# Optimization experiments

Measured on AMD Instinct MI355X. Metric: run time of the kernel, lower is better.

Reference implementation:

```python
import jax, jax.numpy as jnp
import numpy as np
import itertools

# ---- fixed problem dims ----
B, C, G, D, H, W_SP = 2, 32, 24, 24, 24, 24   # octahedral group |G| = 24 (isomorphic to S4)
N_SEL = 3                                      # selective bispectrum: 2nd shift restricted to {e, transposition, 4-cycle}
FEAT = G * N_SEL                               # 72 invariant features per channel
HEAD = 64


def _octahedral_tables():
    """Cayley table of the octahedral rotation group (== S4) and the selective generator set."""
    perms = list(itertools.permutations(range(4)))          # lexicographic; identity at index 0
    idx = {p: i for i, p in enumerate(perms)}
    # cayley[i, j] = index of p_i o p_j, with (p o q)(k) = p(q(k))
    cay = np.array([[idx[tuple(p[q[k]] for k in range(4))] for q in perms] for p in perms],
                   dtype=np.int32)
    sel = np.array([idx[(0, 1, 2, 3)],   # identity
                    idx[(1, 0, 2, 3)],   # transposition (generator)
                    idx[(1, 2, 3, 0)]],  # 4-cycle (generator)
                   dtype=np.int32)
    return cay, sel


def setup_inputs() -> dict:
    key = jax.random.key(0)
    k1, k2, k3 = jax.random.split(key, 3)
    x = jax.random.normal(k1, (B, C, G, D, H, W_SP), dtype=jnp.float32)
    cay, sel = _octahedral_tables()
    # 1x1x1 Conv3d params: weight (HEAD, C*FEAT), bias (HEAD,)
    fan_in = C * FEAT
    W = jax.random.normal(k2, (HEAD, fan_in), dtype=jnp.float32) * (1.0 / np.sqrt(fan_in))
    b = jax.random.normal(k3, (HEAD,), dtype=jnp.float32) * 0.01
    return {"x": x, "W": W, "b": b,
            "cayley": jnp.asarray(cay), "sel_idx": jnp.asarray(sel)}


def _bispectrum_pool(x, W, b, cayley, sel_idx):
    Bb, Cc, Gg, Dd, Hh, Ww = x.shape
    # (B,C,G,D,H,W) -> rows of group signals, one per (b,c,voxel)
    xf = x.astype(jnp.float32).transpose(0, 1, 3, 4, 5, 2).reshape(-1, Gg)   # (N, 24)
    N = xf.shape[0]
    # Selective triple correlation (bispectrum in group domain):
    #   tau[n, h, s] = sum_g f(g) * f(g.h) * f(g.s),  s in selective generator set
    tau = jnp.zeros((N, Gg, N_SEL), dtype=jnp.float32)
    for g in range(Gg):                      # fixed small loop over 24 group elements
        row = cayley[g]                      # (24,) indices of g.h for all h
        fgh = xf[:, row]                     # (N, 24)
        fgs = fgh[:, sel_idx]                # (N, 3)
        tau = tau + xf[:, g][:, None, None] * fgh[:, :, None] * fgs[:, None, :]
    beta = tau.reshape(N, FEAT)              # real part of the bispectrum
    # sign * log1p compression
    out = jnp.sign(beta) * jnp.log1p(jnp.abs(beta))
    # (N, FEAT) -> (B, C*FEAT, D, H, W), channel index = c*FEAT + f (matches torch permute/reshape)
    out = out.reshape(Bb, Cc, Dd, Hh, Ww, FEAT).transpose(0, 1, 5, 2, 3, 4)
    out = out.reshape(Bb, Cc * FEAT, Dd, Hh, Ww)
    out = jax.nn.relu(out)
    # 1x1x1 conv == per-voxel GEMM
    y = jnp.einsum('bkdhw,ok->bodhw', out, W) + b[None, :, None, None, None]
    return y


def reference(x, W, b, cayley, sel_idx):
    return _bispectrum_pool(x, W, b, cayley, sel_idx)
```

## Files before the change

kernel.cpp:

```cpp
#include <hip/hip_runtime.h>
#include <stdint.h>

#define DHW         13824
#define NCH         32
#define NG          24
#define KDIM        2304
#define NHEAD       64
#define TP          16
#define CHS         16
#define FPC         64
#define KP2         2048
#define KS2         64
#define KPSTG       32
#define KQ          8
#define KPE         1032
#define TILES_PER_B 864
#define NTILES      1728
#define OUTN        1769472
#define PREPB       512
#define FILLB       1728

typedef __attribute__((ext_vector_type(2))) float    f32x2;
typedef __attribute__((ext_vector_type(8))) short    s16x8;
typedef __attribute__((ext_vector_type(4))) float    f32x4;
typedef __attribute__((ext_vector_type(4))) uint32_t u32x4;

struct Tables { int cay[NG][NG]; int s1[NG]; int s2[NG]; int t1h[NG]; int rep[12]; };

constexpr Tables make_tables() {
    int perms[NG][4] = {};
    int n = 0;
    for (int a = 0; a < 4; ++a)
        for (int b = 0; b < 4; ++b) {
            if (b == a) continue;
            for (int c = 0; c < 4; ++c) {
                if (c == a || c == b) continue;
                int d = 6 - a - b - c;
                perms[n][0] = a; perms[n][1] = b; perms[n][2] = c; perms[n][3] = d;
                ++n;
            }
        }
    int si1 = 0, si2 = 0;
    for (int i = 0; i < NG; ++i) {
        if (perms[i][0] == 1 && perms[i][1] == 0 && perms[i][2] == 2 && perms[i][3] == 3) si1 = i;
        if (perms[i][0] == 1 && perms[i][1] == 2 && perms[i][2] == 3 && perms[i][3] == 0) si2 = i;
    }
    Tables t{};
    for (int p = 0; p < NG; ++p) {
        for (int q = 0; q < NG; ++q) {
            int c0 = perms[p][perms[q][0]];
            int c1 = perms[p][perms[q][1]];
            int c2 = perms[p][perms[q][2]];
            int c3 = perms[p][perms[q][3]];
            int r = 0;
            for (int i = 0; i < NG; ++i)
                if (perms[i][0] == c0 && perms[i][1] == c1 &&
                    perms[i][2] == c2 && perms[i][3] == c3) { r = i; break; }
            t.cay[p][q] = r;
        }
        t.s1[p] = t.cay[p][si1];
        t.s2[p] = t.cay[p][si2];
    }
    for (int h = 0; h < NG; ++h) t.t1h[h] = t.cay[si1][h];
    int nr = 0;
    for (int h = 0; h < NG; ++h) if (h < t.t1h[h]) t.rep[nr++] = h;
    return t;
}
constexpr Tables TAB = make_tables();

__device__ __forceinline__ uint32_t f2bf(float f) {
    uint32_t u = __float_as_uint(f);
    u += 0x7fffu + ((u >> 16) & 1u);
    return u >> 16;
}

__global__ __launch_bounds__(256) void init_all(const float* __restrict__ W,
                                                unsigned short* __restrict__ WbS,
                                                const float* __restrict__ bias,
                                                float* __restrict__ y) {
    const int blk = blockIdx.x;
    if (blk < PREPB) {
        int i = blk * 256 + threadIdx.x;
        int j  = i & 7;
        int t1_ = i >> 3;
        int l  = t1_ & 63;
        int t2_ = t1_ >> 6;
        int kk = t2_ & (KS2 - 1);
        int ot = t2_ >> 6;
        int o = ot * 16 + (l & 15);
        int k = kk * 32 + ((l >> 4) << 3) + j;
        int stage = k >> 10;
        int q     = k & 1023;
        int c = stage * CHS + (q >> 6);
        int f = q & 63;
        const float* Wo = W + o * KDIM + c * 72;
        float val = 0.f;
        if (f < 24)      val = Wo[f * 3 + 0];
        else if (f < 36) { int h = TAB.rep[f - 24];
                           val = Wo[h * 3 + 1] + Wo[TAB.t1h[h] * 3 + 1]; }
        else if (f < 60) { int h = f - 36;          val = Wo[h * 3 + 2]; }
        WbS[i] = (unsigned short)f2bf(val * 0.69314718055994531f);
    } else {
        const int i4 = (blk - PREPB) * 256 + threadIdx.x;
        const float b = bias[((i4 * 4) / DHW) & (NHEAD - 1)];
        f32x4 v; v[0] = b; v[1] = b; v[2] = b; v[3] = b;
        ((f32x4*)y)[i4] = v;
    }
}

__global__ __launch_bounds__(256, 2)
void bispec_fused(
        const float* __restrict__ x,
        const unsigned short* __restrict__ WbS,
        float* __restrict__ y)
{
    __shared__ alignas(16) unsigned short featS[TP * KPE];

    const int bid = blockIdx.x;
    const int NB  = NTILES * 2;
    const int swz   = (bid & 7) * (NB / 8) + (bid >> 3);
    const int tile  = swz % NTILES;
    const int stage = swz / NTILES;
    const int bb  = tile / TILES_PER_B;
    const int psp = (tile - bb * TILES_PER_B) * TP;
    const int tid = threadIdx.x;

    const int p0 = tid & 15;
    const int cl = tid >> 4;
    const int w  = tid >> 6;
    const int l  = tid & 63;
    const int ln = l & 15;
    const int lh = l >> 4;

    f32x4 accA = {0.f, 0.f, 0.f, 0.f};
    f32x4 accB = {0.f, 0.f, 0.f, 0.f};
    f32x4 accC = {0.f, 0.f, 0.f, 0.f};
    f32x4 accD = {0.f, 0.f, 0.f, 0.f};

    {
        const int c0 = stage * CHS + cl;
        const unsigned idx0 = (unsigned)(bb * NCH + c0) * (NG * DHW) + (unsigned)(psp + p0);
        float xf[NG];
        #pragma unroll
        for (int g = 0; g < NG; ++g) xf[g] = x[idx0 + (unsigned)(g * DHW)];

        f32x2 tau02[NG];
        float tau1[12];
        #pragma unroll
        for (int h = 0; h < NG; ++h) tau02[h] = (f32x2){0.f, 0.f};
        #pragma unroll
        for (int r = 0; r < 12; ++r) tau1[r] = 0.f;
        #pragma unroll
        for (int g = 0; g < NG; ++g) {
            const float xg = xf[g];
            const f32x2 q02 = (f32x2){xg, xg} * (f32x2){xg, xf[TAB.s2[g]]};
            const float q1 = xg * xf[TAB.s1[g]];
            #pragma unroll
            for (int h = 0; h < NG; ++h) {
                const float v = xf[TAB.cay[g][h]];
                tau02[h] = __builtin_elementwise_fma((f32x2){v, v}, q02, tau02[h]);
            }
            #pragma unroll
            for (int r = 0; r < 12; ++r) {
                const float v = xf[TAB.cay[g][TAB.rep[r]]];
                tau1[r] = fmaf(q1, v, tau1[r]);
            }
        }
        uint32_t pk[FPC / 2];
        #pragma unroll
        for (int i = 0; i < 12; ++i) {
            float a = __log2f(1.f + fmaxf(tau02[2*i][0],   0.f));
            float b = __log2f(1.f + fmaxf(tau02[2*i+1][0], 0.f));
            pk[i] = f2bf(a) | (f2bf(b) << 16);
        }
        #pragma unroll
        for (int i = 0; i < 6; ++i) {
            float a = __log2f(1.f + fmaxf(tau1[2*i],   0.f));
            float b = __log2f(1.f + fmaxf(tau1[2*i+1], 0.f));
            pk[12 + i] = f2bf(a) | (f2bf(b) << 16);
        }
        #pragma unroll
        for (int i = 0; i < 12; ++i) {
            float a = __log2f(1.f + fmaxf(tau02[2*i][1],   0.f));
            float b = __log2f(1.f + fmaxf(tau02[2*i+1][1], 0.f));
            pk[18 + i] = f2bf(a) | (f2bf(b) << 16);
        }
        pk[30] = 0u; pk[31] = 0u;
        uint32_t* dst = (uint32_t*)&featS[p0 * KPE + cl * FPC];
        #pragma unroll
        for (int i = 0; i < FPC / 2; i += 4) {
            u32x4 v; v[0] = pk[i]; v[1] = pk[i+1]; v[2] = pk[i+2]; v[3] = pk[i+3];
            *(u32x4*)(dst + i) = v;
        }
    }
    __syncthreads();

    {
        const unsigned kb = (unsigned)(stage * KPSTG + w * KQ);
        const unsigned short* fb = &featS[ln * KPE + (w * KQ) * 32 + lh * 8];
        const s16x8* wb = (const s16x8*)WbS;

        s16x8 bc = *(const s16x8*)(fb);
        #pragma unroll
        for (int kk = 0; kk < KQ; ++kk) {
            s16x8 bn = bc;
            if (kk + 1 < KQ) bn = *(const s16x8*)(fb + (kk + 1) * 32);
            const unsigned ai = (kb + (unsigned)kk) * 64u + (unsigned)l;
            s16x8 a0 = wb[ai];
            s16x8 a1 = wb[ai + 1u * KS2 * 64u];
            s16x8 a2 = wb[ai + 2u * KS2 * 64u];
            s16x8 a3 = wb[ai + 3u * KS2 * 64u];
            accA = __builtin_amdgcn_mfma_f32_16x16x32_bf16(a0, bc, accA, 0, 0, 0);
            accB = __builtin_amdgcn_mfma_f32_16x16x32_bf16(a1, bc, accB, 0, 0, 0);
            accC = __builtin_amdgcn_mfma_f32_16x16x32_bf16(a2, bc, accC, 0, 0, 0);
            accD = __builtin_amdgcn_mfma_f32_16x16x32_bf16(a3, bc, accD, 0, 0, 0);
            bc = bn;
        }
    }
    __syncthreads();

    f32x4* redS = (f32x4*)featS;
    redS[(w * 4 + 0) * 64 + l] = accA;
    redS[(w * 4 + 1) * 64 + l] = accB;
    redS[(w * 4 + 2) * 64 + l] = accC;
    redS[(w * 4 + 3) * 64 + l] = accD;
    __syncthreads();
    f32x4 r = redS[(0 * 4 + w) * 64 + l] + redS[(1 * 4 + w) * 64 + l]
            + redS[(2 * 4 + w) * 64 + l] + redS[(3 * 4 + w) * 64 + l];

    const size_t obase = (size_t)bb * NHEAD * DHW + (size_t)(psp + ln);
    #pragma unroll
    for (int j = 0; j < 4; ++j) {
        const int o = w * 16 + lh * 4 + j;
        atomicAdd(&y[obase + (size_t)o * DHW], r[j]);
    }
}

extern "C" void kernel_launch(void* const* d_in, const int* in_sizes, int n_in,
                              void* d_out, int out_size, void* d_ws, size_t ws_size,
                              hipStream_t stream) {
    const float* x    = (const float*)d_in[0];
    const float* W    = (const float*)d_in[1];
    const float* bias = (const float*)d_in[2];
    unsigned short* WbS = (unsigned short*)d_ws;
    float* y = (float*)d_out;

    init_all<<<dim3(PREPB + FILLB), dim3(256), 0, stream>>>(W, WbS, bias, y);
    bispec_fused<<<dim3(NTILES * 2), dim3(256), 0, stream>>>(x, WbS, y);
}
```

Before: 57.64 us.

## Convert fused bispectrum kernel to persistent work-queue with next-tile prefetch

The one-block-per-tile launch becomes a persistent grid of 1024 blocks that take work items from a global atomic counter, reset in the init kernel. While the MFMA GEMM runs on the current tile, each thread loads the next tile's 24 group values into registers, so global load latency can overlap with compute. This removes per-block launch and tail costs, but it adds an atomic plus barrier per item, extra register pressure from the prefetch buffer, and it drops the earlier L2-friendly swizzle ordering.

```diff
diff --git a/kernel.cpp b/kernel.cpp
--- a/kernel.cpp
+++ b/kernel.cpp
@@ -16,9 +16,12 @@
 #define KPE         1032
 #define TILES_PER_B 864
 #define NTILES      1728
+#define NITEMS      (NTILES * 2)
+#define GRIDP       1024
 #define OUTN        1769472
 #define PREPB       512
 #define FILLB       1728
+#define WS_WBS      294912
 
 typedef __attribute__((ext_vector_type(2))) float    f32x2;
 typedef __attribute__((ext_vector_type(8))) short    s16x8;
@@ -77,8 +80,10 @@
 __global__ __launch_bounds__(256) void init_all(const float* __restrict__ W,
                                                 unsigned short* __restrict__ WbS,
                                                 const float* __restrict__ bias,
-                                                float* __restrict__ y) {
+                                                float* __restrict__ y,
+                                                unsigned* __restrict__ qcnt) {
     const int blk = blockIdx.x;
+    if (blk == 0 && threadIdx.x == 0) *qcnt = 0u;
     if (blk < PREPB) {
         int i = blk * 256 + threadIdx.x;
         int j  = i & 7;
@@ -112,19 +117,13 @@
 void bispec_fused(
         const float* __restrict__ x,
         const unsigned short* __restrict__ WbS,
-        float* __restrict__ y)
+        float* __restrict__ y,
+        unsigned* __restrict__ qcnt)
 {
     __shared__ alignas(16) unsigned short featS[TP * KPE];
-
-    const int bid = blockIdx.x;
-    const int NB  = NTILES * 2;
-    const int swz   = (bid & 7) * (NB / 8) + (bid >> 3);
-    const int tile  = swz % NTILES;
-    const int stage = swz / NTILES;
-    const int bb  = tile / TILES_PER_B;
-    const int psp = (tile - bb * TILES_PER_B) * TP;
+    __shared__ unsigned sIdx;
+
     const int tid = threadIdx.x;
-
     const int p0 = tid & 15;
     const int cl = tid >> 4;
     const int w  = tid >> 6;
@@ -132,107 +131,144 @@
     const int ln = l & 15;
     const int lh = l >> 4;
 
-    f32x4 accA = {0.f, 0.f, 0.f, 0.f};
-    f32x4 accB = {0.f, 0.f, 0.f, 0.f};
-    f32x4 accC = {0.f, 0.f, 0.f, 0.f};
-    f32x4 accD = {0.f, 0.f, 0.f, 0.f};
-
+    if (tid == 0) sIdx = atomicAdd(qcnt, 1u);
+    __syncthreads();
+    unsigned item = sIdx;
+    if (item >= NITEMS) return;
+
+    unsigned tile  = item % NTILES;
+    unsigned stage = item / NTILES;
+    unsigned bb  = tile / TILES_PER_B;
+    unsigned psp = (tile - bb * TILES_PER_B) * TP;
+    float xf[NG];
     {
-        const int c0 = stage * CHS + cl;
-        const unsigned idx0 = (unsigned)(bb * NCH + c0) * (NG * DHW) + (unsigned)(psp + p0);
-        float xf[NG];
+        const unsigned idx0 = (bb * NCH + stage * CHS + (unsigned)cl) * (NG * DHW)
+                            + (psp + (unsigned)p0);
         #pragma unroll
         for (int g = 0; g < NG; ++g) xf[g] = x[idx0 + (unsigned)(g * DHW)];
-
-        f32x2 tau02[NG];
-        float tau1[12];
+    }
+
+    for (;;) {
+        const unsigned cur_bb = bb, cur_psp = psp, cur_stage = stage;
+
+        {
+            f32x2 tau02[NG];
+            float tau1[12];
+            #pragma unroll
+            for (int h = 0; h < NG; ++h) tau02[h] = (f32x2){0.f, 0.f};
+            #pragma unroll
+            for (int r = 0; r < 12; ++r) tau1[r] = 0.f;
+            #pragma unroll
+            for (int g = 0; g < NG; ++g) {
+                const float xg = xf[g];
+                const f32x2 q02 = (f32x2){xg, xg} * (f32x2){xg, xf[TAB.s2[g]]};
+                const float q1 = xg * xf[TAB.s1[g]];
+                #pragma unroll
+                for (int h = 0; h < NG; ++h) {
+                    const float v = xf[TAB.cay[g][h]];
+                    tau02[h] = __builtin_elementwise_fma((f32x2){v, v}, q02, tau02[h]);
+                }
+                #pragma unroll
+                for (int r = 0; r < 12; ++r) {
+                    const float v = xf[TAB.cay[g][TAB.rep[r]]];
+                    tau1[r] = fmaf(q1, v, tau1[r]);
+                }
+            }
+            uint32_t pk[FPC / 2];
+            #pragma unroll
+            for (int i = 0; i < 12; ++i) {
+                float a = __log2f(1.f + fmaxf(tau02[2*i][0],   0.f));
+                float b = __log2f(1.f + fmaxf(tau02[2*i+1][0], 0.f));
+                pk[i] = f2bf(a) | (f2bf(b) << 16);
+            }
+            #pragma unroll
+            for (int i = 0; i < 6; ++i) {
+                float a = __log2f(1.f + fmaxf(tau1[2*i],   0.f));
+                float b = __log2f(1.f + fmaxf(tau1[2*i+1], 0.f));
+                pk[12 + i] = f2bf(a) | (f2bf(b) << 16);
+            }
+            #pragma unroll
+            for (int i = 0; i < 12; ++i) {
+                float a = __log2f(1.f + fmaxf(tau02[2*i][1],   0.f));
+                float b = __log2f(1.f + fmaxf(tau02[2*i+1][1], 0.f));
+                pk[18 + i] = f2bf(a) | (f2bf(b) << 16);
+            }
+            pk[30] = 0u; pk[31] = 0u;
+            uint32_t* dst = (uint32_t*)&featS[p0 * KPE + cl * FPC];
+            #pragma unroll
+            for (int i = 0; i < FPC / 2; i += 4) {
+                u32x4 v; v[0] = pk[i]; v[1] = pk[i+1]; v[2] = pk[i+2]; v[3] = pk[i+3];
+                *(u32x4*)(dst + i) = v;
+            }
+        }
+
+        if (tid == 0) sIdx = atomicAdd(qcnt, 1u);
+        __syncthreads();
+        const unsigned nitem = sIdx;
+        const bool have_next = (nitem < NITEMS);
+
+        float xn[NG];
+        if (have_next) {
+            tile  = nitem % NTILES;
+            stage = nitem / NTILES;
+            bb  = tile / TILES_PER_B;
+            psp = (tile - bb * TILES_PER_B) * TP;
+            const unsigned nidx0 = (bb * NCH + stage * CHS + (unsigned)cl) * (NG * DHW)
+                                 + (psp + (unsigned)p0);
+            #pragma unroll
+            for (int g = 0; g < NG; ++g) xn[g] = x[nidx0 + (unsigned)(g * DHW)];
+        }
+
+        f32x4 accA = {0.f, 0.f, 0.f, 0.f};
+        f32x4 accB = {0.f, 0.f, 0.f, 0.f};
+        f32x4 accC = {0.f, 0.f, 0.f, 0.f};
+        f32x4 accD = {0.f, 0.f, 0.f, 0.f};
+        {
+            const unsigned kb = cur_stage * KPSTG + (unsigned)(w * KQ);
+            const unsigned short* fb = &featS[ln * KPE + (w * KQ) * 32 + lh * 8];
+            const s16x8* wb = (const s16x8*)WbS;
+
+            s16x8 bc = *(const s16x8*)(fb);
+            #pragma unroll
+            for (int kk = 0; kk < KQ; ++kk) {
+                s16x8 bn = bc;
+                if (kk + 1 < KQ) bn = *(const s16x8*)(fb + (kk + 1) * 32);
+                const unsigned ai = (kb + (unsigned)kk) * 64u + (unsigned)l;
+                s16x8 a0 = wb[ai];
+                s16x8 a1 = wb[ai + 1u * KS2 * 64u];
+                s16x8 a2 = wb[ai + 2u * KS2 * 64u];
+                s16x8 a3 = wb[ai + 3u * KS2 * 64u];
+                accA = __builtin_amdgcn_mfma_f32_16x16x32_bf16(a0, bc, accA, 0, 0, 0);
+                accB = __builtin_amdgcn_mfma_f32_16x16x32_bf16(a1, bc, accB, 0, 0, 0);
+                accC = __builtin_amdgcn_mfma_f32_16x16x32_bf16(a2, bc, accC, 0, 0, 0);
+                accD = __builtin_amdgcn_mfma_f32_16x16x32_bf16(a3, bc, accD, 0, 0, 0);
+                bc = bn;
+            }
+        }
+        __syncthreads();
+
+        {
+            f32x4* redS = (f32x4*)featS;
+            redS[(w * 4 + 0) * 64 + l] = accA;
+            redS[(w * 4 + 1) * 64 + l] = accB;
+            redS[(w * 4 + 2) * 64 + l] = accC;
+            redS[(w * 4 + 3) * 64 + l] = accD;
+            __syncthreads();
+            f32x4 r = redS[(0 * 4 + w) * 64 + l] + redS[(1 * 4 + w) * 64 + l]
+                    + redS[(2 * 4 + w) * 64 + l] + redS[(3 * 4 + w) * 64 + l];
+
+            const size_t obase = (size_t)cur_bb * NHEAD * DHW + (size_t)(cur_psp + ln);
+            #pragma unroll
+            for (int j = 0; j < 4; ++j) {
+                const int o = w * 16 + lh * 4 + j;
+                atomicAdd(&y[obase + (size_t)o * DHW], r[j]);
+            }
+        }
+        __syncthreads();
+
+        if (!have_next) break;
         #pragma unroll
-        for (int h = 0; h < NG; ++h) tau02[h] = (f32x2){0.f, 0.f};
-        #pragma unroll
-        for (int r = 0; r < 12; ++r) tau1[r] = 0.f;
-        #pragma unroll
-        for (int g = 0; g < NG; ++g) {
-            const float xg = xf[g];
-            const f32x2 q02 = (f32x2){xg, xg} * (f32x2){xg, xf[TAB.s2[g]]};
-            const float q1 = xg * xf[TAB.s1[g]];
-            #pragma unroll
-            for (int h = 0; h < NG; ++h) {
-                const float v = xf[TAB.cay[g][h]];
-                tau02[h] = __builtin_elementwise_fma((f32x2){v, v}, q02, tau02[h]);
-            }
-            #pragma unroll
-            for (int r = 0; r < 12; ++r) {
-                const float v = xf[TAB.cay[g][TAB.rep[r]]];
-                tau1[r] = fmaf(q1, v, tau1[r]);
-            }
-        }
-        uint32_t pk[FPC / 2];
-        #pragma unroll
-        for (int i = 0; i < 12; ++i) {
-            float a = __log2f(1.f + fmaxf(tau02[2*i][0],   0.f));
-            float b = __log2f(1.f + fmaxf(tau02[2*i+1][0], 0.f));
-            pk[i] = f2bf(a) | (f2bf(b) << 16);
-        }
-        #pragma unroll
-        for (int i = 0; i < 6; ++i) {
-            float a = __log2f(1.f + fmaxf(tau1[2*i],   0.f));
-            float b = __log2f(1.f + fmaxf(tau1[2*i+1], 0.f));
-            pk[12 + i] = f2bf(a) | (f2bf(b) << 16);
-        }
-        #pragma unroll
-        for (int i = 0; i < 12; ++i) {
-            float a = __log2f(1.f + fmaxf(tau02[2*i][1],   0.f));
-            float b = __log2f(1.f + fmaxf(tau02[2*i+1][1], 0.f));
-            pk[18 + i] = f2bf(a) | (f2bf(b) << 16);
-        }
-        pk[30] = 0u; pk[31] = 0u;
-        uint32_t* dst = (uint32_t*)&featS[p0 * KPE + cl * FPC];
-        #pragma unroll
-        for (int i = 0; i < FPC / 2; i += 4) {
-            u32x4 v; v[0] = pk[i]; v[1] = pk[i+1]; v[2] = pk[i+2]; v[3] = pk[i+3];
-            *(u32x4*)(dst + i) = v;
-        }
-    }
-    __syncthreads();
-
-    {
-        const unsigned kb = (unsigned)(stage * KPSTG + w * KQ);
-        const unsigned short* fb = &featS[ln * KPE + (w * KQ) * 32 + lh * 8];
-        const s16x8* wb = (const s16x8*)WbS;
-
-        s16x8 bc = *(const s16x8*)(fb);
-        #pragma unroll
-        for (int kk = 0; kk < KQ; ++kk) {
-            s16x8 bn = bc;
-            if (kk + 1 < KQ) bn = *(const s16x8*)(fb + (kk + 1) * 32);
-            const unsigned ai = (kb + (unsigned)kk) * 64u + (unsigned)l;
-            s16x8 a0 = wb[ai];
-            s16x8 a1 = wb[ai + 1u * KS2 * 64u];
-            s16x8 a2 = wb[ai + 2u * KS2 * 64u];
-            s16x8 a3 = wb[ai + 3u * KS2 * 64u];
-            accA = __builtin_amdgcn_mfma_f32_16x16x32_bf16(a0, bc, accA, 0, 0, 0);
-            accB = __builtin_amdgcn_mfma_f32_16x16x32_bf16(a1, bc, accB, 0, 0, 0);
-            accC = __builtin_amdgcn_mfma_f32_16x16x32_bf16(a2, bc, accC, 0, 0, 0);
-            accD = __builtin_amdgcn_mfma_f32_16x16x32_bf16(a3, bc, accD, 0, 0, 0);
-            bc = bn;
-        }
-    }
-    __syncthreads();
-
-    f32x4* redS = (f32x4*)featS;
-    redS[(w * 4 + 0) * 64 + l] = accA;
-    redS[(w * 4 + 1) * 64 + l] = accB;
-    redS[(w * 4 + 2) * 64 + l] = accC;
-    redS[(w * 4 + 3) * 64 + l] = accD;
-    __syncthreads();
-    f32x4 r = redS[(0 * 4 + w) * 64 + l] + redS[(1 * 4 + w) * 64 + l]
-            + redS[(2 * 4 + w) * 64 + l] + redS[(3 * 4 + w) * 64 + l];
-
-    const size_t obase = (size_t)bb * NHEAD * DHW + (size_t)(psp + ln);
-    #pragma unroll
-    for (int j = 0; j < 4; ++j) {
-        const int o = w * 16 + lh * 4 + j;
-        atomicAdd(&y[obase + (size_t)o * DHW], r[j]);
+        for (int g = 0; g < NG; ++g) xf[g] = xn[g];
     }
 }
 
@@ -243,8 +279,9 @@
     const float* W    = (const float*)d_in[1];
     const float* bias = (const float*)d_in[2];
     unsigned short* WbS = (unsigned short*)d_ws;
+    unsigned* qcnt = (unsigned*)((char*)d_ws + WS_WBS);
     float* y = (float*)d_out;
 
-    init_all<<<dim3(PREPB + FILLB), dim3(256), 0, stream>>>(W, WbS, bias, y);
-    bispec_fused<<<dim3(NTILES * 2), dim3(256), 0, stream>>>(x, WbS, y);
-}
+    init_all<<<dim3(PREPB + FILLB), dim3(256), 0, stream>>>(W, WbS, bias, y, qcnt);
+    bispec_fused<<<dim3(GRIDP), dim3(256), 0, stream>>>(x, WbS, y, qcnt);
+}
```

Result: slower. 75.79 us (+31.5%).
